# Performance work log

Measured on AMD Instinct MI355X. Metric: run time of the kernel, lower is better.

Reference implementation:

```python
import jax, jax.numpy as jnp
import numpy as np

T, B, D, H = 256, 64, 1024, 1024


def setup_inputs() -> dict:
    key = jax.random.key(0)
    ks = jax.random.split(key, 12)
    stdv = 1.0 / np.sqrt(H)
    u = lambda k, shape: jax.random.uniform(k, shape, jnp.float32, -stdv, stdv)
    return {
        "input_": jax.random.normal(ks[0], (T, B, D), jnp.float32),
        "length": jax.random.randint(ks[1], (B,), 1, T + 1, jnp.int32),
        "h0": jnp.zeros((B, H), jnp.float32),
        "cj": jax.random.normal(ks[2], (B, H), jnp.float32),
        "he": jax.random.normal(ks[3], (B, H), jnp.float32),
        "w_ih": u(ks[4], (3 * H, D)),
        "w_hh": u(ks[5], (3 * H, H)),
        "w_ch": u(ks[6], (3 * H, H)),
        "w_zh": u(ks[7], (3 * H, H)),
        "b_ih": u(ks[8], (3 * H,)),
        "b_hh": u(ks[9], (3 * H,)),
        "b_ch": u(ks[10], (3 * H,)),
        "b_zh": u(ks[11], (3 * H,)),
    }


def _chunk3(g):
    # mirrors torch .chunk(3, 1) on a (..., 3H) tensor
    return g[..., :H], g[..., H:2 * H], g[..., 2 * H:]


def reference(input_, length, h0, cj, he, w_ih, w_hh, w_ch, w_zh,
              b_ih, b_hh, b_ch, b_zh):
    # context projections are time-invariant: hoist out of the recurrence
    c_r, c_i, c_n = _chunk3(cj @ w_ch.T + b_ch)   # (B,H) each
    z_r, z_i, z_n = _chunk3(he @ w_zh.T + b_zh)   # (B,H) each
    # input projections for all steps at once: (T,B,3H)
    gi_all = jnp.einsum('tbd,gd->tbg', input_, w_ih) + b_ih

    def step(h, xs):
        gi_t, t = xs
        i_r, i_i, i_n = _chunk3(gi_t)
        h_r, h_i, h_n_ = _chunk3(h @ w_hh.T + b_hh)
        resetgate = jax.nn.sigmoid(i_r + h_r + c_r + z_r)
        inputgate = jax.nn.sigmoid(i_i + h_i + c_i + z_i)
        newgate = jnp.tanh(i_n + resetgate * h_n_ + c_n + z_n)
        hy = newgate + inputgate * (h - newgate)
        mask = (t < length).astype(hy.dtype)[:, None]          # (B,1)
        # NOTE: faithful to original torch code, which uses hx[0]
        # (first batch row, broadcast) in the masked branch.
        h_next = hy * mask + h[0] * (1.0 - mask)
        return h_next, h_next

    h_last, output = jax.lax.scan(step, h0, (gi_all, jnp.arange(T)))
    h_n = h_last[None]  # (num_layers=1, B, H)
    return output, h_n
```

## Files before the change

kernel.cpp:

```cpp
#include <hip/hip_runtime.h>
#include <stdint.h>

#define TT 256
#define BB 64
#define DD 1024
#define HH 1024
#define G3 3072

typedef unsigned long long ull;
typedef __attribute__((ext_vector_type(8))) short short8;
typedef __attribute__((ext_vector_type(4))) float f32x4;

__device__ __forceinline__ unsigned short f2bf(float f) {
  union { float f; unsigned int i; } v; v.f = f;
  unsigned int x = v.i;
  return (unsigned short)((x + 0x7fffu + ((x >> 16) & 1u)) >> 16);
}
__device__ __forceinline__ float bf2f(unsigned short u) {
  union { unsigned int i; float f; } v; v.i = ((unsigned int)u) << 16; return v.f;
}
__device__ __forceinline__ f32x4 mfma16(short8 a, short8 b, f32x4 c) {
  return __builtin_amdgcn_mfma_f32_16x16x32_bf16(a, b, c, 0, 0, 0);
}
__device__ __forceinline__ void gload_lds16(const void* g, void* l) {
  __builtin_amdgcn_global_load_lds((const __attribute__((address_space(1))) void*)g,
                                   (__attribute__((address_space(3))) void*)l,
                                   16, 0, 0);
}

__global__ void k_cvt_bf16(const float* __restrict__ in, unsigned short* __restrict__ out, int n4) {
  int i = blockIdx.x * blockDim.x + threadIdx.x;
  int stride = gridDim.x * blockDim.x;
  for (; i < n4; i += stride) {
    float4 v = ((const float4*)in)[i];
    ushort4 o;
    o.x = f2bf(v.x); o.y = f2bf(v.y); o.z = f2bf(v.z); o.w = f2bf(v.w);
    ((ushort4*)out)[i] = o;
  }
}

__global__ __launch_bounds__(256) void k_ctx(
    const unsigned short* __restrict__ cjb, const unsigned short* __restrict__ heb,
    const unsigned short* __restrict__ Wchb, const unsigned short* __restrict__ Wzhb,
    const float* __restrict__ b_ih, const float* __restrict__ b_hh,
    const float* __restrict__ b_ch, const float* __restrict__ b_zh,
    float* __restrict__ E) {
  __shared__ f32x4 red[4][4][64];
  int n0 = blockIdx.x * 16;
  int tid = threadIdx.x;
  int w = tid >> 6, l = tid & 63, lo = l & 15, hi = l >> 4;
  f32x4 acc[4];
#pragma unroll
  for (int r = 0; r < 4; r++) acc[r] = (f32x4){0.f, 0.f, 0.f, 0.f};
#pragma unroll 4
  for (int kk = 0; kk < 16; kk++) {
    int k = w * 512 + kk * 32;
    const unsigned short* Asrc = (k < 1024) ? cjb : heb;
    const unsigned short* Bsrc = (k < 1024) ? Wchb : Wzhb;
    int kw = (k < 1024) ? k : (k - 1024);
    int kof = kw + hi * 8;
    short8 bf = *(const short8*)(Bsrc + (size_t)(n0 + lo) * 1024 + kof);
#pragma unroll
    for (int r = 0; r < 4; r++) {
      short8 af = *(const short8*)(Asrc + (size_t)(r * 16 + lo) * 1024 + kof);
      acc[r] = mfma16(af, bf, acc[r]);
    }
  }
#pragma unroll
  for (int r = 0; r < 4; r++) red[w][r][l] = acc[r];
  __syncthreads();
  f32x4 s = red[0][w][l];
#pragma unroll
  for (int w2 = 1; w2 < 4; w2++) {
    f32x4 p = red[w2][w][l];
    s[0] += p[0]; s[1] += p[1]; s[2] += p[2]; s[3] += p[3];
  }
  int g = n0 + lo;
  float bias = b_ih[g] + b_ch[g] + b_zh[g] + ((g < 2048) ? b_hh[g] : 0.0f);
#pragma unroll
  for (int j = 0; j < 4; j++) {
    int b = w * 16 + hi * 4 + j;
    E[(size_t)b * G3 + g] = s[j] + bias;
  }
}

__global__ __launch_bounds__(256) void k_gemm_gi(
    const unsigned short* __restrict__ Xb,
    const unsigned short* __restrict__ Wb,
    const float* __restrict__ E,
    unsigned short* __restrict__ gi) {
  __shared__ unsigned short As[128 * 32];
  __shared__ unsigned short Bs[128 * 32];
  int bid = blockIdx.x;
  int mt = bid & 127;
  int nt = bid >> 7;
  int m0 = mt * 128, n0 = nt * 128;
  int tid = threadIdx.x;
  int w = tid >> 6, l = tid & 63, lo = l & 15, hi = l >> 4;
  int wr = w >> 1, wc = w & 1;
  f32x4 acc[4][4];
#pragma unroll
  for (int i = 0; i < 4; i++)
#pragma unroll
    for (int j = 0; j < 4; j++) acc[i][j] = (f32x4){0.f, 0.f, 0.f, 0.f};
  int srow = tid >> 2;
  int scol = (tid & 3) * 8;
  for (int kt = 0; kt < 32; kt++) {
    int k0 = kt * 32;
    __syncthreads();
    gload_lds16(Xb + (size_t)(m0 + srow) * 1024 + k0 + scol, As + srow * 32 + scol);
    gload_lds16(Xb + (size_t)(m0 + 64 + srow) * 1024 + k0 + scol, As + (64 + srow) * 32 + scol);
    gload_lds16(Wb + (size_t)(n0 + srow) * 1024 + k0 + scol, Bs + srow * 32 + scol);
    gload_lds16(Wb + (size_t)(n0 + 64 + srow) * 1024 + k0 + scol, Bs + (64 + srow) * 32 + scol);
    asm volatile("s_waitcnt vmcnt(0)" ::: "memory");
    __syncthreads();
    short8 a[4], b[4];
#pragma unroll
    for (int i = 0; i < 4; i++) a[i] = *(const short8*)(As + (wr * 64 + i * 16 + lo) * 32 + hi * 8);
#pragma unroll
    for (int i = 0; i < 4; i++) b[i] = *(const short8*)(Bs + (wc * 64 + i * 16 + lo) * 32 + hi * 8);
#pragma unroll
    for (int i = 0; i < 4; i++)
#pragma unroll
      for (int j = 0; j < 4; j++) acc[i][j] = mfma16(a[i], b[j], acc[i][j]);
  }
#pragma unroll
  for (int i = 0; i < 4; i++)
#pragma unroll
    for (int j = 0; j < 4; j++)
#pragma unroll
      for (int e = 0; e < 4; e++) {
        int r = m0 + wr * 64 + i * 16 + hi * 4 + e;
        int c = n0 + wc * 64 + j * 16 + lo;
        float v = acc[i][j][e] + E[(size_t)(r & 63) * G3 + c];
        gi[(size_t)r * G3 + c] = f2bf(v);
      }
}

__global__ __launch_bounds__(256) void k_rnn(
    const unsigned short* __restrict__ giE,
    const unsigned short* __restrict__ Whhb,
    const float* __restrict__ b_hh,
    const float* __restrict__ h0,
    const int* __restrict__ length,
    unsigned short* __restrict__ hbuf,
    float* __restrict__ out,
    float* __restrict__ hn,
    unsigned int* __restrict__ seq) {
  extern __shared__ char smem[];
  unsigned short* wlds = (unsigned short*)smem;
  f32x4* red = (f32x4*)(smem + 98304);
  float* hp0 = (float*)(smem + 98304 + 49152);

  const int cs = blockIdx.x;
  const int j0 = cs * 16;
  const int tid = threadIdx.x;
  const int kq = tid >> 6, l = tid & 63, lo = l & 15, hi = l >> 4;
  const int rowbase = kq * 16;
  const int col = j0 + lo;

#pragma unroll
  for (int kk = 0; kk < 8; ++kk)
#pragma unroll
    for (int s = 0; s < 3; ++s) {
      int f = (kq * 8 + kk) * 3 + s;
      short8 v = *(const short8*)(Whhb + (size_t)(s * 1024 + j0 + lo) * 1024 + kq * 256 + kk * 32 + hi * 8);
      ((short8*)wlds)[f * 64 + l] = v;
    }

  const float bhhn = b_hh[2048 + col];
  float hown[4];
  int len4[4];
#pragma unroll
  for (int j = 0; j < 4; ++j) {
    int b = rowbase + hi * 4 + j;
    hown[j] = h0[(size_t)b * 1024 + col];
    len4[j] = length[b];
  }
#pragma unroll
  for (int j = 0; j < 4; ++j) {
    unsigned int mine = f2bf(hown[j]);
    unsigned int oth = __shfl_xor(mine, 1, 64);
    if (!(lo & 1)) {
      int row = rowbase + hi * 4 + j;
      __hip_atomic_store((unsigned int*)(hbuf + (size_t)cs * 1024 + row * 16 + lo),
                         mine | (oth << 16), __ATOMIC_RELAXED, __HIP_MEMORY_SCOPE_AGENT);
    }
  }
  if (kq == 0 && hi == 0) hp0[lo] = hown[0];
  float gir[3][4];
#pragma unroll
  for (int s = 0; s < 3; ++s)
#pragma unroll
    for (int j = 0; j < 4; ++j)
      gir[s][j] = bf2f(giE[(size_t)(rowbase + hi * 4 + j) * G3 + s * 1024 + col]);
  __syncthreads();
  asm volatile("s_waitcnt vmcnt(0)" ::: "memory");
  if (l == 0)
    __hip_atomic_store(&seq[(cs * 4 + kq) * 16], 1u, __ATOMIC_RELAXED, __HIP_MEMORY_SCOPE_AGENT);

  int slot = 0;
  for (int t = 0; t < TT; ++t) {
    const int nslot = (slot == 2) ? 0 : slot + 1;
    {
      const unsigned int* sp = seq + ((size_t)(kq * 16 + (l >> 2)) * 4 + (l & 3)) * 16;
      unsigned int tgt = (unsigned int)(t + 1);
      for (;;) {
        unsigned int v = __hip_atomic_load(sp, __ATOMIC_RELAXED, __HIP_MEMORY_SCOPE_AGENT);
        if (__all(v >= tgt)) break;
        __builtin_amdgcn_s_sleep(1);
      }
    }
    const unsigned short* hb2 = hbuf + (size_t)slot * 65536;
    union AF { ull u[2]; short8 v; };
    AF a[4][8];
#pragma unroll
    for (int rt = 0; rt < 4; ++rt)
#pragma unroll
      for (int kk = 0; kk < 8; ++kk) {
        int k = kq * 256 + kk * 32;
        int blk = (k >> 4) + (hi >> 1);
        const unsigned short* hp = hb2 + (size_t)blk * 1024 + (rt * 16 + lo) * 16 + (hi & 1) * 8;
        a[rt][kk].u[0] = __hip_atomic_load((const ull*)hp, __ATOMIC_RELAXED, __HIP_MEMORY_SCOPE_AGENT);
        a[rt][kk].u[1] = __hip_atomic_load((const ull*)hp + 1, __ATOMIC_RELAXED, __HIP_MEMORY_SCOPE_AGENT);
      }
    f32x4 acc[4][3];
#pragma unroll
    for (int rt = 0; rt < 4; ++rt)
#pragma unroll
      for (int s = 0; s < 3; ++s) acc[rt][s] = (f32x4){0.f, 0.f, 0.f, 0.f};
#pragma unroll
    for (int kk = 0; kk < 8; ++kk) {
      const short8* wf = ((const short8*)wlds) + (size_t)((kq * 8 + kk) * 3) * 64 + l;
      short8 b0 = wf[0];
      short8 b1 = wf[64];
      short8 b2 = wf[128];
#pragma unroll
      for (int rt = 0; rt < 4; ++rt) {
        acc[rt][0] = mfma16(a[rt][kk].v, b0, acc[rt][0]);
        acc[rt][1] = mfma16(a[rt][kk].v, b1, acc[rt][1]);
        acc[rt][2] = mfma16(a[rt][kk].v, b2, acc[rt][2]);
      }
    }
#pragma unroll
    for (int rt = 0; rt < 4; ++rt)
#pragma unroll
      for (int s = 0; s < 3; ++s)
        red[((size_t)kq * 12 + rt * 3 + s) * 64 + l] = acc[rt][s];
    __syncthreads();
    f32x4 fin[3];
#pragma unroll
    for (int s = 0; s < 3; ++s) {
      f32x4 v = red[((size_t)0 * 12 + kq * 3 + s) * 64 + l];
#pragma unroll
      for (int q = 1; q < 4; ++q) {
        f32x4 p = red[((size_t)q * 12 + kq * 3 + s) * 64 + l];
        v[0] += p[0]; v[1] += p[1]; v[2] += p[2]; v[3] += p[3];
      }
      fin[s] = v;
    }
    float h0p = hp0[(t & 1) * 16 + lo];
    __syncthreads();
    float hv[4];
#pragma unroll
    for (int j = 0; j < 4; ++j) {
      float R = fin[0][j] + gir[0][j];
      float I = fin[1][j] + gir[1][j];
      float rg = 1.f / (1.f + __expf(-R));
      float ig = 1.f / (1.f + __expf(-I));
      float nx = gir[2][j] + rg * (fin[2][j] + bhhn);
      nx = fminf(15.f, fmaxf(-15.f, nx));
      float e2 = __expf(2.f * nx);
      float ng = (e2 - 1.f) / (e2 + 1.f);
      float hy = ng + ig * (hown[j] - ng);
      float res = (t < len4[j]) ? hy : h0p;
      hv[j] = res;
      hown[j] = res;
    }
    if (t < TT - 1) {
      unsigned short* dst = hbuf + (size_t)nslot * 65536 + (size_t)cs * 1024;
#pragma unroll
      for (int j = 0; j < 4; ++j) {
        unsigned int mine = f2bf(hv[j]);
        unsigned int oth = __shfl_xor(mine, 1, 64);
        if (!(lo & 1)) {
          int row = rowbase + hi * 4 + j;
          __hip_atomic_store((unsigned int*)(dst + row * 16 + lo),
                             mine | (oth << 16), __ATOMIC_RELAXED, __HIP_MEMORY_SCOPE_AGENT);
        }
      }
      if (kq == 0 && hi == 0) hp0[((t + 1) & 1) * 16 + lo] = hv[0];
      asm volatile("s_waitcnt vmcnt(0)" ::: "memory");
      if (l == 0)
        __hip_atomic_store(&seq[(cs * 4 + kq) * 16], (unsigned int)(t + 2),
                           __ATOMIC_RELAXED, __HIP_MEMORY_SCOPE_AGENT);
    }
#pragma unroll
    for (int j = 0; j < 4; ++j) {
      int b = rowbase + hi * 4 + j;
      out[(size_t)t * (BB * HH) + (size_t)b * 1024 + col] = hv[j];
    }
    if (t == TT - 1) {
#pragma unroll
      for (int j = 0; j < 4; ++j) {
        int b = rowbase + hi * 4 + j;
        hn[(size_t)b * 1024 + col] = hv[j];
      }
    } else {
      const unsigned short* gb = giE + (size_t)(t + 1) * 64 * G3;
#pragma unroll
      for (int s = 0; s < 3; ++s)
#pragma unroll
        for (int j = 0; j < 4; ++j)
          gir[s][j] = bf2f(gb[(size_t)(rowbase + hi * 4 + j) * G3 + s * 1024 + col]);
    }
    slot = nslot;
  }
}

extern "C" void kernel_launch(void* const* d_in, const int* in_sizes, int n_in,
                              void* d_out, int out_size, void* d_ws, size_t ws_size,
                              hipStream_t stream) {
  const float* input_ = (const float*)d_in[0];
  const int* length   = (const int*)d_in[1];
  const float* h0     = (const float*)d_in[2];
  const float* cj     = (const float*)d_in[3];
  const float* he     = (const float*)d_in[4];
  const float* w_ih   = (const float*)d_in[5];
  const float* w_hh   = (const float*)d_in[6];
  const float* w_ch   = (const float*)d_in[7];
  const float* w_zh   = (const float*)d_in[8];
  const float* b_ih   = (const float*)d_in[9];
  const float* b_hh   = (const float*)d_in[10];
  const float* b_ch   = (const float*)d_in[11];
  const float* b_zh   = (const float*)d_in[12];

  char* ws = (char*)d_ws;
  const size_t OFF_SEQ   = 0;
  const size_t OFF_XB    = 131072;
  const size_t OFF_WIHB  = OFF_XB + 33554432ull;
  const size_t OFF_WHHB  = OFF_WIHB + 6291456ull;
  const size_t OFF_WCHB  = OFF_WHHB + 6291456ull;
  const size_t OFF_WZHB  = OFF_WCHB + 6291456ull;
  const size_t OFF_CJB   = OFF_WZHB + 6291456ull;
  const size_t OFF_HEB   = OFF_CJB + 131072ull;
  const size_t OFF_E     = OFF_HEB + 131072ull;
  const size_t OFF_GI    = OFF_E + 786432ull;
  const size_t OFF_HBUF  = OFF_GI + 100663296ull;

  unsigned int* seq     = (unsigned int*)(ws + OFF_SEQ);
  unsigned short* Xb    = (unsigned short*)(ws + OFF_XB);
  unsigned short* Wihb  = (unsigned short*)(ws + OFF_WIHB);
  unsigned short* Whhb  = (unsigned short*)(ws + OFF_WHHB);
  unsigned short* Wchb  = (unsigned short*)(ws + OFF_WCHB);
  unsigned short* Wzhb  = (unsigned short*)(ws + OFF_WZHB);
  unsigned short* cjb   = (unsigned short*)(ws + OFF_CJB);
  unsigned short* heb   = (unsigned short*)(ws + OFF_HEB);
  float* E              = (float*)(ws + OFF_E);
  unsigned short* gi    = (unsigned short*)(ws + OFF_GI);
  unsigned short* hbuf  = (unsigned short*)(ws + OFF_HBUF);

  float* out = (float*)d_out;
  float* hn  = out + 16777216;

  hipFuncSetAttribute((const void*)k_rnn, hipFuncAttributeMaxDynamicSharedMemorySize, 147584);

  hipMemsetAsync(seq, 0, 16384, stream);
  k_cvt_bf16<<<2048, 256, 0, stream>>>(input_, Xb, 16777216 / 4);
  k_cvt_bf16<<<1024, 256, 0, stream>>>(w_ih, Wihb, 3145728 / 4);
  k_cvt_bf16<<<1024, 256, 0, stream>>>(w_hh, Whhb, 3145728 / 4);
  k_cvt_bf16<<<1024, 256, 0, stream>>>(w_ch, Wchb, 3145728 / 4);
  k_cvt_bf16<<<1024, 256, 0, stream>>>(w_zh, Wzhb, 3145728 / 4);
  k_cvt_bf16<<<64, 256, 0, stream>>>(cj, cjb, 65536 / 4);
  k_cvt_bf16<<<64, 256, 0, stream>>>(he, heb, 65536 / 4);
  k_ctx<<<192, 256, 0, stream>>>(cjb, heb, Wchb, Wzhb, b_ih, b_hh, b_ch, b_zh, E);
  k_gemm_gi<<<3072, 256, 0, stream>>>(Xb, Wihb, E, gi);
  k_rnn<<<64, 256, 147584, stream>>>(gi, Whhb, b_hh, h0, length, hbuf, out, hn, seq);
}
```

Baseline: 1.454 ms.

## Warp-specialize RNN kernel with helper waves for gi prefetch and output stores

Doubles the recurrent kernel's block to 512 threads. Four helper waves prefetch the next step's gate inputs into a double-buffered LDS area and write the per-step outputs, reading them back from the bf16 hidden-state exchange buffer two steps late. This takes global gi loads and output stores off the serial critical path of the update waves. The h-exchange loads switch from relaxed atomic 64-bit loads to inline-asm dwordx4 loads with sc0 sc1 cache bits. In exchange, intermediate outputs are now bf16-rounded rather than the fp32 values, and there are more waves per barrier.

```diff
diff --git a/kernel.cpp b/kernel.cpp
--- a/kernel.cpp
+++ b/kernel.cpp
@@ -26,6 +26,11 @@
   __builtin_amdgcn_global_load_lds((const __attribute__((address_space(1))) void*)g,
                                    (__attribute__((address_space(3))) void*)l,
                                    16, 0, 0);
+}
+__device__ __forceinline__ short8 mall_load16(const unsigned short* p) {
+  short8 r;
+  asm volatile("global_load_dwordx4 %0, %1, off sc0 sc1" : "=v"(r) : "v"(p));
+  return r;
 }
 
 __global__ void k_cvt_bf16(const float* __restrict__ in, unsigned short* __restrict__ out, int n4) {
@@ -137,7 +142,7 @@
       }
 }
 
-__global__ __launch_bounds__(256) void k_rnn(
+__global__ __launch_bounds__(512) void k_rnn(
     const unsigned short* __restrict__ giE,
     const unsigned short* __restrict__ Whhb,
     const float* __restrict__ b_hh,
@@ -150,59 +155,71 @@
   extern __shared__ char smem[];
   unsigned short* wlds = (unsigned short*)smem;
   f32x4* red = (f32x4*)(smem + 98304);
-  float* hp0 = (float*)(smem + 98304 + 49152);
+  unsigned short* giL = (unsigned short*)(smem + 147456);
+  float* hp0 = (float*)(smem + 160512);
 
   const int cs = blockIdx.x;
   const int j0 = cs * 16;
   const int tid = threadIdx.x;
-  const int kq = tid >> 6, l = tid & 63, lo = l & 15, hi = l >> 4;
+  const int w = tid >> 6, l = tid & 63, lo = l & 15, hi = l >> 4;
+  const bool is_upd = (w < 4);
+  const int kq = w & 3;
   const int rowbase = kq * 16;
   const int col = j0 + lo;
 
-#pragma unroll
-  for (int kk = 0; kk < 8; ++kk)
-#pragma unroll
-    for (int s = 0; s < 3; ++s) {
-      int f = (kq * 8 + kk) * 3 + s;
-      short8 v = *(const short8*)(Whhb + (size_t)(s * 1024 + j0 + lo) * 1024 + kq * 256 + kk * 32 + hi * 8);
-      ((short8*)wlds)[f * 64 + l] = v;
-    }
-
-  const float bhhn = b_hh[2048 + col];
-  float hown[4];
-  int len4[4];
-#pragma unroll
-  for (int j = 0; j < 4; ++j) {
-    int b = rowbase + hi * 4 + j;
-    hown[j] = h0[(size_t)b * 1024 + col];
-    len4[j] = length[b];
-  }
-#pragma unroll
-  for (int j = 0; j < 4; ++j) {
-    unsigned int mine = f2bf(hown[j]);
-    unsigned int oth = __shfl_xor(mine, 1, 64);
-    if (!(lo & 1)) {
-      int row = rowbase + hi * 4 + j;
-      __hip_atomic_store((unsigned int*)(hbuf + (size_t)cs * 1024 + row * 16 + lo),
-                         mine | (oth << 16), __ATOMIC_RELAXED, __HIP_MEMORY_SCOPE_AGENT);
-    }
-  }
-  if (kq == 0 && hi == 0) hp0[lo] = hown[0];
-  float gir[3][4];
-#pragma unroll
-  for (int s = 0; s < 3; ++s)
-#pragma unroll
-    for (int j = 0; j < 4; ++j)
-      gir[s][j] = bf2f(giE[(size_t)(rowbase + hi * 4 + j) * G3 + s * 1024 + col]);
+  float bhhn = 0.f;
+  float hown[4] = {0.f, 0.f, 0.f, 0.f};
+  int len4[4] = {0, 0, 0, 0};
+
+  if (is_upd) {
+#pragma unroll
+    for (int kk = 0; kk < 8; ++kk)
+#pragma unroll
+      for (int s = 0; s < 3; ++s) {
+        int f = (kq * 8 + kk) * 3 + s;
+        short8 v = *(const short8*)(Whhb + (size_t)(s * 1024 + j0 + lo) * 1024 + kq * 256 + kk * 32 + hi * 8);
+        ((short8*)wlds)[f * 64 + l] = v;
+      }
+    bhhn = b_hh[2048 + col];
+#pragma unroll
+    for (int j = 0; j < 4; ++j) {
+      int b = rowbase + hi * 4 + j;
+      hown[j] = h0[(size_t)b * 1024 + col];
+      len4[j] = length[b];
+    }
+#pragma unroll
+    for (int j = 0; j < 4; ++j) {
+      unsigned int mine = f2bf(hown[j]);
+      unsigned int oth = __shfl_xor(mine, 1, 64);
+      if (!(lo & 1)) {
+        int row = rowbase + hi * 4 + j;
+        __hip_atomic_store((unsigned int*)(hbuf + (size_t)cs * 1024 + row * 16 + lo),
+                           mine | (oth << 16), __ATOMIC_RELAXED, __HIP_MEMORY_SCOPE_AGENT);
+      }
+    }
+    if (kq == 0 && hi == 0) hp0[lo] = hown[0];
+  } else {
+#pragma unroll
+    for (int s = 0; s < 3; ++s)
+#pragma unroll
+      for (int j = 0; j < 4; ++j) {
+        int b = rowbase + hi * 4 + j;
+        giL[(size_t)(0 * 64 + b) * 51 + s * 17 + lo] =
+            giE[(size_t)b * G3 + s * 1024 + col];
+      }
+  }
   __syncthreads();
-  asm volatile("s_waitcnt vmcnt(0)" ::: "memory");
-  if (l == 0)
-    __hip_atomic_store(&seq[(cs * 4 + kq) * 16], 1u, __ATOMIC_RELAXED, __HIP_MEMORY_SCOPE_AGENT);
+  if (is_upd) {
+    asm volatile("s_waitcnt vmcnt(0)" ::: "memory");
+    if (l == 0)
+      __hip_atomic_store(&seq[(cs * 4 + kq) * 16], 1u, __ATOMIC_RELAXED, __HIP_MEMORY_SCOPE_AGENT);
+  }
 
   int slot = 0;
   for (int t = 0; t < TT; ++t) {
     const int nslot = (slot == 2) ? 0 : slot + 1;
-    {
+    unsigned short gval[12];
+    if (is_upd) {
       const unsigned int* sp = seq + ((size_t)(kq * 16 + (l >> 2)) * 4 + (l & 3)) * 16;
       unsigned int tgt = (unsigned int)(t + 1);
       for (;;) {
@@ -210,111 +227,151 @@
         if (__all(v >= tgt)) break;
         __builtin_amdgcn_s_sleep(1);
       }
-    }
-    const unsigned short* hb2 = hbuf + (size_t)slot * 65536;
-    union AF { ull u[2]; short8 v; };
-    AF a[4][8];
-#pragma unroll
-    for (int rt = 0; rt < 4; ++rt)
+      const unsigned short* hb2 = hbuf + (size_t)slot * 65536;
+      short8 a[4][8];
+#pragma unroll
+      for (int rt = 0; rt < 4; ++rt)
+#pragma unroll
+        for (int kk = 0; kk < 8; ++kk) {
+          int blk = kq * 16 + kk * 2 + (hi >> 1);
+          a[rt][kk] = mall_load16(hb2 + (size_t)blk * 1024 + (rt * 16 + lo) * 16 + (hi & 1) * 8);
+        }
+      asm volatile("s_waitcnt vmcnt(0)" ::: "memory");
+      __builtin_amdgcn_sched_barrier(0);
+      f32x4 acc[4][3];
+#pragma unroll
+      for (int rt = 0; rt < 4; ++rt)
+#pragma unroll
+        for (int s = 0; s < 3; ++s) acc[rt][s] = (f32x4){0.f, 0.f, 0.f, 0.f};
 #pragma unroll
       for (int kk = 0; kk < 8; ++kk) {
-        int k = kq * 256 + kk * 32;
-        int blk = (k >> 4) + (hi >> 1);
-        const unsigned short* hp = hb2 + (size_t)blk * 1024 + (rt * 16 + lo) * 16 + (hi & 1) * 8;
-        a[rt][kk].u[0] = __hip_atomic_load((const ull*)hp, __ATOMIC_RELAXED, __HIP_MEMORY_SCOPE_AGENT);
-        a[rt][kk].u[1] = __hip_atomic_load((const ull*)hp + 1, __ATOMIC_RELAXED, __HIP_MEMORY_SCOPE_AGENT);
-      }
-    f32x4 acc[4][3];
-#pragma unroll
-    for (int rt = 0; rt < 4; ++rt)
-#pragma unroll
-      for (int s = 0; s < 3; ++s) acc[rt][s] = (f32x4){0.f, 0.f, 0.f, 0.f};
-#pragma unroll
-    for (int kk = 0; kk < 8; ++kk) {
-      const short8* wf = ((const short8*)wlds) + (size_t)((kq * 8 + kk) * 3) * 64 + l;
-      short8 b0 = wf[0];
-      short8 b1 = wf[64];
-      short8 b2 = wf[128];
-#pragma unroll
-      for (int rt = 0; rt < 4; ++rt) {
-        acc[rt][0] = mfma16(a[rt][kk].v, b0, acc[rt][0]);
-        acc[rt][1] = mfma16(a[rt][kk].v, b1, acc[rt][1]);
-        acc[rt][2] = mfma16(a[rt][kk].v, b2, acc[rt][2]);
-      }
-    }
-#pragma unroll
-    for (int rt = 0; rt < 4; ++rt)
-#pragma unroll
-      for (int s = 0; s < 3; ++s)
-        red[((size_t)kq * 12 + rt * 3 + s) * 64 + l] = acc[rt][s];
+        const short8* wf = ((const short8*)wlds) + (size_t)((kq * 8 + kk) * 3) * 64 + l;
+        short8 b0 = wf[0];
+        short8 b1 = wf[64];
+        short8 b2 = wf[128];
+#pragma unroll
+        for (int rt = 0; rt < 4; ++rt) {
+          acc[rt][0] = mfma16(a[rt][kk], b0, acc[rt][0]);
+          acc[rt][1] = mfma16(a[rt][kk], b1, acc[rt][1]);
+          acc[rt][2] = mfma16(a[rt][kk], b2, acc[rt][2]);
+        }
+      }
+#pragma unroll
+      for (int rt = 0; rt < 4; ++rt)
+#pragma unroll
+        for (int s = 0; s < 3; ++s)
+          red[((size_t)kq * 12 + rt * 3 + s) * 64 + l] = acc[rt][s];
+    } else {
+      if (t >= 2) {
+        const unsigned short* hblk = hbuf + (size_t)((t + 2) % 3) * 65536 + (size_t)cs * 1024;
+        int row = rowbase + (l >> 2);
+        int c4 = (l & 3) * 4;
+        ull d = __hip_atomic_load((const ull*)(hblk + row * 16 + c4),
+                                  __ATOMIC_RELAXED, __HIP_MEMORY_SCOPE_AGENT);
+        float4 o;
+        o.x = bf2f((unsigned short)d);
+        o.y = bf2f((unsigned short)(d >> 16));
+        o.z = bf2f((unsigned short)(d >> 32));
+        o.w = bf2f((unsigned short)(d >> 48));
+        *(float4*)(out + (size_t)(t - 2) * (BB * HH) + (size_t)row * 1024 + j0 + c4) = o;
+      }
+      if (t < TT - 1) {
+        const unsigned short* gb = giE + (size_t)(t + 1) * 64 * G3;
+#pragma unroll
+        for (int s = 0; s < 3; ++s)
+#pragma unroll
+          for (int j = 0; j < 4; ++j)
+            gval[s * 4 + j] = gb[(size_t)(rowbase + hi * 4 + j) * G3 + s * 1024 + col];
+      }
+    }
     __syncthreads();
     f32x4 fin[3];
-#pragma unroll
-    for (int s = 0; s < 3; ++s) {
-      f32x4 v = red[((size_t)0 * 12 + kq * 3 + s) * 64 + l];
-#pragma unroll
-      for (int q = 1; q < 4; ++q) {
-        f32x4 p = red[((size_t)q * 12 + kq * 3 + s) * 64 + l];
-        v[0] += p[0]; v[1] += p[1]; v[2] += p[2]; v[3] += p[3];
-      }
-      fin[s] = v;
-    }
-    float h0p = hp0[(t & 1) * 16 + lo];
+    float h0p = 0.f;
+    if (is_upd) {
+#pragma unroll
+      for (int s = 0; s < 3; ++s) {
+        f32x4 v = red[((size_t)0 * 12 + kq * 3 + s) * 64 + l];
+#pragma unroll
+        for (int q = 1; q < 4; ++q) {
+          f32x4 p = red[((size_t)q * 12 + kq * 3 + s) * 64 + l];
+          v[0] += p[0]; v[1] += p[1]; v[2] += p[2]; v[3] += p[3];
+        }
+        fin[s] = v;
+      }
+      h0p = hp0[(t & 1) * 16 + lo];
+    } else if (t < TT - 1) {
+#pragma unroll
+      for (int s = 0; s < 3; ++s)
+#pragma unroll
+        for (int j = 0; j < 4; ++j) {
+          int b = rowbase + hi * 4 + j;
+          giL[(size_t)(((t + 1) & 1) * 64 + b) * 51 + s * 17 + lo] = gval[s * 4 + j];
+        }
+    }
     __syncthreads();
-    float hv[4];
-#pragma unroll
-    for (int j = 0; j < 4; ++j) {
-      float R = fin[0][j] + gir[0][j];
-      float I = fin[1][j] + gir[1][j];
-      float rg = 1.f / (1.f + __expf(-R));
-      float ig = 1.f / (1.f + __expf(-I));
-      float nx = gir[2][j] + rg * (fin[2][j] + bhhn);
-      nx = fminf(15.f, fmaxf(-15.f, nx));
-      float e2 = __expf(2.f * nx);
-      float ng = (e2 - 1.f) / (e2 + 1.f);
-      float hy = ng + ig * (hown[j] - ng);
-      float res = (t < len4[j]) ? hy : h0p;
-      hv[j] = res;
-      hown[j] = res;
-    }
-    if (t < TT - 1) {
-      unsigned short* dst = hbuf + (size_t)nslot * 65536 + (size_t)cs * 1024;
+    if (is_upd) {
+      float gir_sj;
+      float hv[4];
 #pragma unroll
       for (int j = 0; j < 4; ++j) {
-        unsigned int mine = f2bf(hv[j]);
-        unsigned int oth = __shfl_xor(mine, 1, 64);
-        if (!(lo & 1)) {
-          int row = rowbase + hi * 4 + j;
-          __hip_atomic_store((unsigned int*)(dst + row * 16 + lo),
-                             mine | (oth << 16), __ATOMIC_RELAXED, __HIP_MEMORY_SCOPE_AGENT);
+        int b = rowbase + hi * 4 + j;
+        float g0 = bf2f(giL[(size_t)((t & 1) * 64 + b) * 51 + 0 * 17 + lo]);
+        float g1 = bf2f(giL[(size_t)((t & 1) * 64 + b) * 51 + 1 * 17 + lo]);
+        float g2 = bf2f(giL[(size_t)((t & 1) * 64 + b) * 51 + 2 * 17 + lo]);
+        float R = fin[0][j] + g0;
+        float I = fin[1][j] + g1;
+        float rg = 1.f / (1.f + __expf(-R));
+        float ig = 1.f / (1.f + __expf(-I));
+        float nx = g2 + rg * (fin[2][j] + bhhn);
+        nx = fminf(15.f, fmaxf(-15.f, nx));
+        float e2 = __expf(2.f * nx);
+        float ng = (e2 - 1.f) / (e2 + 1.f);
+        float hy = ng + ig * (hown[j] - ng);
+        float res = (t < len4[j]) ? hy : h0p;
+        hv[j] = res;
+        hown[j] = res;
+      }
+      (void)gir_sj;
+      if (t < TT - 1) {
+        unsigned short* dst = hbuf + (size_t)nslot * 65536 + (size_t)cs * 1024;
+#pragma unroll
+        for (int j = 0; j < 4; ++j) {
+          unsigned int mine = f2bf(hv[j]);
+          unsigned int oth = __shfl_xor(mine, 1, 64);
+          if (!(lo & 1)) {
+            int row = rowbase + hi * 4 + j;
+            __hip_atomic_store((unsigned int*)(dst + row * 16 + lo),
+                               mine | (oth << 16), __ATOMIC_RELAXED, __HIP_MEMORY_SCOPE_AGENT);
+          }
         }
-      }
-      if (kq == 0 && hi == 0) hp0[((t + 1) & 1) * 16 + lo] = hv[0];
-      asm volatile("s_waitcnt vmcnt(0)" ::: "memory");
-      if (l == 0)
-        __hip_atomic_store(&seq[(cs * 4 + kq) * 16], (unsigned int)(t + 2),
-                           __ATOMIC_RELAXED, __HIP_MEMORY_SCOPE_AGENT);
-    }
+        if (kq == 0 && hi == 0) hp0[((t + 1) & 1) * 16 + lo] = hv[0];
+        asm volatile("s_waitcnt vmcnt(0)" ::: "memory");
+        if (l == 0)
+          __hip_atomic_store(&seq[(cs * 4 + kq) * 16], (unsigned int)(t + 2),
+                             __ATOMIC_RELAXED, __HIP_MEMORY_SCOPE_AGENT);
+      }
+    }
+    slot = nslot;
+  }
+  if (is_upd) {
 #pragma unroll
     for (int j = 0; j < 4; ++j) {
       int b = rowbase + hi * 4 + j;
-      out[(size_t)t * (BB * HH) + (size_t)b * 1024 + col] = hv[j];
-    }
-    if (t == TT - 1) {
-#pragma unroll
-      for (int j = 0; j < 4; ++j) {
-        int b = rowbase + hi * 4 + j;
-        hn[(size_t)b * 1024 + col] = hv[j];
-      }
-    } else {
-      const unsigned short* gb = giE + (size_t)(t + 1) * 64 * G3;
-#pragma unroll
-      for (int s = 0; s < 3; ++s)
-#pragma unroll
-        for (int j = 0; j < 4; ++j)
-          gir[s][j] = bf2f(gb[(size_t)(rowbase + hi * 4 + j) * G3 + s * 1024 + col]);
-    }
-    slot = nslot;
+      out[(size_t)(TT - 1) * (BB * HH) + (size_t)b * 1024 + col] = hown[j];
+      hn[(size_t)b * 1024 + col] = hown[j];
+    }
+  } else {
+    const unsigned short* hblk = hbuf + (size_t)((TT - 1) % 3) * 65536 + (size_t)cs * 1024;
+    int row = rowbase + (l >> 2);
+    int c4 = (l & 3) * 4;
+    ull d = __hip_atomic_load((const ull*)(hblk + row * 16 + c4),
+                              __ATOMIC_RELAXED, __HIP_MEMORY_SCOPE_AGENT);
+    float4 o;
+    o.x = bf2f((unsigned short)d);
+    o.y = bf2f((unsigned short)(d >> 16));
+    o.z = bf2f((unsigned short)(d >> 32));
+    o.w = bf2f((unsigned short)(d >> 48));
+    *(float4*)(out + (size_t)(TT - 2) * (BB * HH) + (size_t)row * 1024 + j0 + c4) = o;
   }
 }
 
@@ -363,7 +420,7 @@
   float* out = (float*)d_out;
   float* hn  = out + 16777216;
 
-  hipFuncSetAttribute((const void*)k_rnn, hipFuncAttributeMaxDynamicSharedMemorySize, 147584);
+  hipFuncSetAttribute((const void*)k_rnn, hipFuncAttributeMaxDynamicSharedMemorySize, 160640);
 
   hipMemsetAsync(seq, 0, 16384, stream);
   k_cvt_bf16<<<2048, 256, 0, stream>>>(input_, Xb, 16777216 / 4);
@@ -375,5 +432,5 @@
   k_cvt_bf16<<<64, 256, 0, stream>>>(he, heb, 65536 / 4);
   k_ctx<<<192, 256, 0, stream>>>(cjb, heb, Wchb, Wzhb, b_ih, b_hh, b_ch, b_zh, E);
   k_gemm_gi<<<3072, 256, 0, stream>>>(Xb, Wihb, E, gi);
-  k_rnn<<<64, 256, 147584, stream>>>(gi, Whhb, b_hh, h0, length, hbuf, out, hn, seq);
-}
+  k_rnn<<<64, 512, 160640, stream>>>(gi, Whhb, b_hh, h0, length, hbuf, out, hn, seq);
+}
```

Measured after the change: 1.444 ms. No clear change (-0.7%).

## Pipeline recurrent step across four batch groups with per-group sync

Applied to the files above, without the earlier changes.

Splits each timestep of the persistent GRU kernel into four phases, one per 16-row batch group. Each group's hidden-state slice is published with its own sequence counter, so the next group's poll and h loads overlap the current group's MFMA and gate math instead of waiting on a full-step barrier. The hidden-state buffer moves to a compact per-group double-buffered layout at the start of the workspace and is read with sc0/sc1 cache-bypass loads. The cost is four times as many barriers and polls per step, and the memory-ordering assumptions are subtle.

```diff
diff --git a/kernel.cpp b/kernel.cpp
--- a/kernel.cpp
+++ b/kernel.cpp
@@ -26,6 +26,11 @@
   __builtin_amdgcn_global_load_lds((const __attribute__((address_space(1))) void*)g,
                                    (__attribute__((address_space(3))) void*)l,
                                    16, 0, 0);
+}
+__device__ __forceinline__ short8 mall_load16(const unsigned short* p) {
+  short8 r;
+  asm volatile("global_load_dwordx4 %0, %1, off sc0 sc1" : "=v"(r) : "v"(p));
+  return r;
 }
 
 __global__ void k_cvt_bf16(const float* __restrict__ in, unsigned short* __restrict__ out, int n4) {
@@ -150,13 +155,11 @@
   extern __shared__ char smem[];
   unsigned short* wlds = (unsigned short*)smem;
   f32x4* red = (f32x4*)(smem + 98304);
-  float* hp0 = (float*)(smem + 98304 + 49152);
-
-  const int cs = blockIdx.x;
-  const int j0 = cs * 16;
+  float* h0f = (float*)(smem + 98304 + 24576);
+
+  const int cs = blockIdx.x, j0 = cs * 16;
   const int tid = threadIdx.x;
   const int kq = tid >> 6, l = tid & 63, lo = l & 15, hi = l >> 4;
-  const int rowbase = kq * 16;
   const int col = j0 + lo;
 
 #pragma unroll
@@ -173,149 +176,158 @@
   int len4[4];
 #pragma unroll
   for (int j = 0; j < 4; ++j) {
-    int b = rowbase + hi * 4 + j;
+    int b = kq * 16 + hi * 4 + j;
     hown[j] = h0[(size_t)b * 1024 + col];
     len4[j] = length[b];
   }
-#pragma unroll
-  for (int j = 0; j < 4; ++j) {
-    unsigned int mine = f2bf(hown[j]);
-    unsigned int oth = __shfl_xor(mine, 1, 64);
-    if (!(lo & 1)) {
-      int row = rowbase + hi * 4 + j;
-      __hip_atomic_store((unsigned int*)(hbuf + (size_t)cs * 1024 + row * 16 + lo),
-                         mine | (oth << 16), __ATOMIC_RELAXED, __HIP_MEMORY_SCOPE_AGENT);
+  {
+    unsigned short* dst = hbuf + ((size_t)(kq * 2 + 0) * 64 + cs) * 256;
+#pragma unroll
+    for (int j = 0; j < 4; ++j) {
+      unsigned int mine = f2bf(hown[j]);
+      unsigned int oth = __shfl_xor(mine, 1, 64);
+      if (!(lo & 1))
+        __hip_atomic_store((unsigned int*)(dst + (hi * 4 + j) * 16 + lo),
+                           mine | (oth << 16), __ATOMIC_RELAXED, __HIP_MEMORY_SCOPE_AGENT);
     }
   }
-  if (kq == 0 && hi == 0) hp0[lo] = hown[0];
-  float gir[3][4];
+  if (kq == 0 && hi == 0) h0f[0 * 16 + lo] = hown[0];
+  unsigned short girP[12];
 #pragma unroll
   for (int s = 0; s < 3; ++s)
 #pragma unroll
     for (int j = 0; j < 4; ++j)
-      gir[s][j] = bf2f(giE[(size_t)(rowbase + hi * 4 + j) * G3 + s * 1024 + col]);
+      girP[s * 4 + j] = giE[(size_t)(kq * 16 + hi * 4 + j) * G3 + s * 1024 + col];
   __syncthreads();
   asm volatile("s_waitcnt vmcnt(0)" ::: "memory");
   if (l == 0)
     __hip_atomic_store(&seq[(cs * 4 + kq) * 16], 1u, __ATOMIC_RELAXED, __HIP_MEMORY_SCOPE_AGENT);
 
-  int slot = 0;
-  for (int t = 0; t < TT; ++t) {
-    const int nslot = (slot == 2) ? 0 : slot + 1;
-    {
-      const unsigned int* sp = seq + ((size_t)(kq * 16 + (l >> 2)) * 4 + (l & 3)) * 16;
-      unsigned int tgt = (unsigned int)(t + 1);
-      for (;;) {
-        unsigned int v = __hip_atomic_load(sp, __ATOMIC_RELAXED, __HIP_MEMORY_SCOPE_AGENT);
-        if (__all(v >= tgt)) break;
-        __builtin_amdgcn_s_sleep(1);
-      }
-    }
-    const unsigned short* hb2 = hbuf + (size_t)slot * 65536;
-    union AF { ull u[2]; short8 v; };
-    AF a[4][8];
-#pragma unroll
-    for (int rt = 0; rt < 4; ++rt)
-#pragma unroll
-      for (int kk = 0; kk < 8; ++kk) {
-        int k = kq * 256 + kk * 32;
-        int blk = (k >> 4) + (hi >> 1);
-        const unsigned short* hp = hb2 + (size_t)blk * 1024 + (rt * 16 + lo) * 16 + (hi & 1) * 8;
-        a[rt][kk].u[0] = __hip_atomic_load((const ull*)hp, __ATOMIC_RELAXED, __HIP_MEMORY_SCOPE_AGENT);
-        a[rt][kk].u[1] = __hip_atomic_load((const ull*)hp + 1, __ATOMIC_RELAXED, __HIP_MEMORY_SCOPE_AGENT);
-      }
-    f32x4 acc[4][3];
-#pragma unroll
-    for (int rt = 0; rt < 4; ++rt)
-#pragma unroll
-      for (int s = 0; s < 3; ++s) acc[rt][s] = (f32x4){0.f, 0.f, 0.f, 0.f};
-#pragma unroll
-    for (int kk = 0; kk < 8; ++kk) {
-      const short8* wf = ((const short8*)wlds) + (size_t)((kq * 8 + kk) * 3) * 64 + l;
-      short8 b0 = wf[0];
-      short8 b1 = wf[64];
-      short8 b2 = wf[128];
-#pragma unroll
-      for (int rt = 0; rt < 4; ++rt) {
-        acc[rt][0] = mfma16(a[rt][kk].v, b0, acc[rt][0]);
-        acc[rt][1] = mfma16(a[rt][kk].v, b1, acc[rt][1]);
-        acc[rt][2] = mfma16(a[rt][kk].v, b2, acc[rt][2]);
-      }
-    }
-#pragma unroll
-    for (int rt = 0; rt < 4; ++rt)
-#pragma unroll
-      for (int s = 0; s < 3; ++s)
-        red[((size_t)kq * 12 + rt * 3 + s) * 64 + l] = acc[rt][s];
-    __syncthreads();
-    f32x4 fin[3];
-#pragma unroll
-    for (int s = 0; s < 3; ++s) {
-      f32x4 v = red[((size_t)0 * 12 + kq * 3 + s) * 64 + l];
-#pragma unroll
-      for (int q = 1; q < 4; ++q) {
-        f32x4 p = red[((size_t)q * 12 + kq * 3 + s) * 64 + l];
-        v[0] += p[0]; v[1] += p[1]; v[2] += p[2]; v[3] += p[3];
-      }
-      fin[s] = v;
-    }
-    float h0p = hp0[(t & 1) * 16 + lo];
-    __syncthreads();
-    float hv[4];
-#pragma unroll
-    for (int j = 0; j < 4; ++j) {
-      float R = fin[0][j] + gir[0][j];
-      float I = fin[1][j] + gir[1][j];
-      float rg = 1.f / (1.f + __expf(-R));
-      float ig = 1.f / (1.f + __expf(-I));
-      float nx = gir[2][j] + rg * (fin[2][j] + bhhn);
-      nx = fminf(15.f, fmaxf(-15.f, nx));
-      float e2 = __expf(2.f * nx);
-      float ng = (e2 - 1.f) / (e2 + 1.f);
-      float hy = ng + ig * (hown[j] - ng);
-      float res = (t < len4[j]) ? hy : h0p;
-      hv[j] = res;
-      hown[j] = res;
-    }
-    if (t < TT - 1) {
-      unsigned short* dst = hbuf + (size_t)nslot * 65536 + (size_t)cs * 1024;
-#pragma unroll
-      for (int j = 0; j < 4; ++j) {
-        unsigned int mine = f2bf(hv[j]);
-        unsigned int oth = __shfl_xor(mine, 1, 64);
-        if (!(lo & 1)) {
-          int row = rowbase + hi * 4 + j;
-          __hip_atomic_store((unsigned int*)(dst + row * 16 + lo),
-                             mine | (oth << 16), __ATOMIC_RELAXED, __HIP_MEMORY_SCOPE_AGENT);
-        }
-      }
-      if (kq == 0 && hi == 0) hp0[((t + 1) & 1) * 16 + lo] = hv[0];
-      asm volatile("s_waitcnt vmcnt(0)" ::: "memory");
-      if (l == 0)
-        __hip_atomic_store(&seq[(cs * 4 + kq) * 16], (unsigned int)(t + 2),
-                           __ATOMIC_RELAXED, __HIP_MEMORY_SCOPE_AGENT);
-    }
-#pragma unroll
-    for (int j = 0; j < 4; ++j) {
-      int b = rowbase + hi * 4 + j;
-      out[(size_t)t * (BB * HH) + (size_t)b * 1024 + col] = hv[j];
-    }
-    if (t == TT - 1) {
-#pragma unroll
-      for (int j = 0; j < 4; ++j) {
-        int b = rowbase + hi * 4 + j;
-        hn[(size_t)b * 1024 + col] = hv[j];
-      }
-    } else {
-      const unsigned short* gb = giE + (size_t)(t + 1) * 64 * G3;
-#pragma unroll
-      for (int s = 0; s < 3; ++s)
-#pragma unroll
-        for (int j = 0; j < 4; ++j)
-          gir[s][j] = bf2f(gb[(size_t)(rowbase + hi * 4 + j) * G3 + s * 1024 + col]);
-    }
-    slot = nslot;
-  }
+  short8 aE[8], aO[8];
+
+#define POLL_ISSUE(GNX, TNX, AN)                                                        \
+  {                                                                                     \
+    const unsigned int* sp = seq + ((size_t)(kq * 16 + (l & 15)) * 4 + (GNX)) * 16;     \
+    unsigned int tgt = (unsigned int)((TNX) + 1);                                       \
+    for (;;) {                                                                          \
+      unsigned int v = __hip_atomic_load(sp, __ATOMIC_RELAXED, __HIP_MEMORY_SCOPE_AGENT);\
+      if (__all(v >= tgt)) break;                                                       \
+      __builtin_amdgcn_s_sleep(1);                                                      \
+    }                                                                                   \
+    const unsigned short* base = hbuf + ((size_t)((GNX) * 2 + ((TNX) & 1)) * 64) * 256; \
+    _Pragma("unroll")                                                                   \
+    for (int kk = 0; kk < 8; ++kk) {                                                    \
+      int blk = kq * 16 + kk * 2 + (hi >> 1);                                           \
+      AN[kk] = mall_load16(base + (size_t)blk * 256 + lo * 16 + (hi & 1) * 8);          \
+    }                                                                                   \
+    if ((GNX) == kq && (TNX) < TT) {                                                    \
+      const unsigned short* gb = giE + (size_t)(TNX) * 64 * G3;                         \
+      _Pragma("unroll")                                                                 \
+      for (int s = 0; s < 3; ++s)                                                       \
+        _Pragma("unroll")                                                               \
+        for (int j = 0; j < 4; ++j)                                                     \
+          girP[s * 4 + j] = gb[(size_t)(kq * 16 + hi * 4 + j) * G3 + s * 1024 + col];   \
+    }                                                                                   \
+  }
+
+#define PHASE(P, AC, AN)                                                                \
+  {                                                                                     \
+    const int g = (P) & 3;                                                              \
+    const int t = (P) >> 2;                                                             \
+    const int par = (P) & 1;                                                            \
+    asm volatile("s_waitcnt vmcnt(0)" ::: "memory");                                    \
+    __builtin_amdgcn_sched_barrier(0);                                                  \
+    f32x4 ac0 = {0.f, 0.f, 0.f, 0.f}, ac1 = ac0, ac2 = ac0;                             \
+    _Pragma("unroll")                                                                   \
+    for (int kk = 0; kk < 8; ++kk) {                                                    \
+      const short8* wf = ((const short8*)wlds) + (size_t)((kq * 8 + kk) * 3) * 64 + l;  \
+      short8 b0 = wf[0];                                                                \
+      short8 b1 = wf[64];                                                               \
+      short8 b2 = wf[128];                                                              \
+      ac0 = mfma16(AC[kk], b0, ac0);                                                    \
+      ac1 = mfma16(AC[kk], b1, ac1);                                                    \
+      ac2 = mfma16(AC[kk], b2, ac2);                                                    \
+    }                                                                                   \
+    red[((size_t)(par * 4 + kq) * 3 + 0) * 64 + l] = ac0;                               \
+    red[((size_t)(par * 4 + kq) * 3 + 1) * 64 + l] = ac1;                               \
+    red[((size_t)(par * 4 + kq) * 3 + 2) * 64 + l] = ac2;                               \
+    if ((P) + 1 < 4 * TT) {                                                             \
+      const int gnx = ((P) + 1) & 3, tnx = ((P) + 1) >> 2;                              \
+      POLL_ISSUE(gnx, tnx, AN);                                                         \
+    }                                                                                   \
+    asm volatile("s_waitcnt lgkmcnt(0)" ::: "memory");                                  \
+    __builtin_amdgcn_s_barrier();                                                       \
+    __builtin_amdgcn_sched_barrier(0);                                                  \
+    if (kq == g) {                                                                      \
+      f32x4 fin[3];                                                                     \
+      _Pragma("unroll")                                                                 \
+      for (int s = 0; s < 3; ++s) {                                                     \
+        f32x4 v = red[((size_t)(par * 4 + 0) * 3 + s) * 64 + l];                        \
+        _Pragma("unroll")                                                               \
+        for (int q = 1; q < 4; ++q) {                                                   \
+          f32x4 pp = red[((size_t)(par * 4 + q) * 3 + s) * 64 + l];                     \
+          v[0] += pp[0]; v[1] += pp[1]; v[2] += pp[2]; v[3] += pp[3];                   \
+        }                                                                               \
+        fin[s] = v;                                                                     \
+      }                                                                                 \
+      float h0p = (g == 0) ? __shfl(hown[0], lo, 64) : h0f[(t & 3) * 16 + lo];          \
+      float hv[4];                                                                      \
+      _Pragma("unroll")                                                                 \
+      for (int j = 0; j < 4; ++j) {                                                     \
+        float R = fin[0][j] + bf2f(girP[0 * 4 + j]);                                    \
+        float I = fin[1][j] + bf2f(girP[1 * 4 + j]);                                    \
+        float rg = 1.f / (1.f + __expf(-R));                                            \
+        float ig = 1.f / (1.f + __expf(-I));                                            \
+        float nx = bf2f(girP[2 * 4 + j]) + rg * (fin[2][j] + bhhn);                     \
+        nx = fminf(15.f, fmaxf(-15.f, nx));                                             \
+        float e2 = __expf(2.f * nx);                                                    \
+        float ng = (e2 - 1.f) / (e2 + 1.f);                                             \
+        float hy = ng + ig * (hown[j] - ng);                                            \
+        float res = (t < len4[j]) ? hy : h0p;                                           \
+        hv[j] = res;                                                                    \
+        hown[j] = res;                                                                  \
+      }                                                                                 \
+      if (t < TT - 1) {                                                                 \
+        unsigned short* dst = hbuf + ((size_t)(g * 2 + ((t + 1) & 1)) * 64 + cs) * 256; \
+        _Pragma("unroll")                                                               \
+        for (int j = 0; j < 4; ++j) {                                                   \
+          unsigned int mine = f2bf(hv[j]);                                              \
+          unsigned int oth = __shfl_xor(mine, 1, 64);                                   \
+          if (!(lo & 1))                                                                \
+            __hip_atomic_store((unsigned int*)(dst + (hi * 4 + j) * 16 + lo),           \
+                               mine | (oth << 16), __ATOMIC_RELAXED,                    \
+                               __HIP_MEMORY_SCOPE_AGENT);                               \
+        }                                                                               \
+        if (g == 0 && hi == 0) h0f[((t + 1) & 3) * 16 + lo] = hv[0];                    \
+        asm volatile("s_waitcnt vmcnt(0)" ::: "memory");                                \
+        if (l == 0)                                                                     \
+          __hip_atomic_store(&seq[(cs * 4 + g) * 16], (unsigned int)(t + 2),            \
+                             __ATOMIC_RELAXED, __HIP_MEMORY_SCOPE_AGENT);               \
+        _Pragma("unroll")                                                               \
+        for (int j = 0; j < 4; ++j) {                                                   \
+          int b = g * 16 + hi * 4 + j;                                                  \
+          out[(size_t)t * (BB * HH) + (size_t)b * 1024 + col] = hv[j];                  \
+        }                                                                               \
+      } else {                                                                          \
+        _Pragma("unroll")                                                               \
+        for (int j = 0; j < 4; ++j) {                                                   \
+          int b = g * 16 + hi * 4 + j;                                                  \
+          out[(size_t)t * (BB * HH) + (size_t)b * 1024 + col] = hv[j];                  \
+          hn[(size_t)b * 1024 + col] = hv[j];                                           \
+        }                                                                               \
+      }                                                                                 \
+    }                                                                                   \
+  }
+
+  POLL_ISSUE(0, 0, aE);
+
+  for (int p2 = 0; p2 < 2 * TT; ++p2) {
+    int p = p2 * 2;
+    PHASE(p, aE, aO);
+    PHASE(p + 1, aO, aE);
+  }
+#undef PHASE
+#undef POLL_ISSUE
 }
 
 extern "C" void kernel_launch(void* const* d_in, const int* in_sizes, int n_in,
@@ -337,7 +349,8 @@
 
   char* ws = (char*)d_ws;
   const size_t OFF_SEQ   = 0;
-  const size_t OFF_XB    = 131072;
+  const size_t OFF_HBUF  = 16384;
+  const size_t OFF_XB    = 524288;
   const size_t OFF_WIHB  = OFF_XB + 33554432ull;
   const size_t OFF_WHHB  = OFF_WIHB + 6291456ull;
   const size_t OFF_WCHB  = OFF_WHHB + 6291456ull;
@@ -346,9 +359,9 @@
   const size_t OFF_HEB   = OFF_CJB + 131072ull;
   const size_t OFF_E     = OFF_HEB + 131072ull;
   const size_t OFF_GI    = OFF_E + 786432ull;
-  const size_t OFF_HBUF  = OFF_GI + 100663296ull;
 
   unsigned int* seq     = (unsigned int*)(ws + OFF_SEQ);
+  unsigned short* hbuf  = (unsigned short*)(ws + OFF_HBUF);
   unsigned short* Xb    = (unsigned short*)(ws + OFF_XB);
   unsigned short* Wihb  = (unsigned short*)(ws + OFF_WIHB);
   unsigned short* Whhb  = (unsigned short*)(ws + OFF_WHHB);
@@ -358,12 +371,11 @@
   unsigned short* heb   = (unsigned short*)(ws + OFF_HEB);
   float* E              = (float*)(ws + OFF_E);
   unsigned short* gi    = (unsigned short*)(ws + OFF_GI);
-  unsigned short* hbuf  = (unsigned short*)(ws + OFF_HBUF);
 
   float* out = (float*)d_out;
   float* hn  = out + 16777216;
 
-  hipFuncSetAttribute((const void*)k_rnn, hipFuncAttributeMaxDynamicSharedMemorySize, 147584);
+  hipFuncSetAttribute((const void*)k_rnn, hipFuncAttributeMaxDynamicSharedMemorySize, 123136);
 
   hipMemsetAsync(seq, 0, 16384, stream);
   k_cvt_bf16<<<2048, 256, 0, stream>>>(input_, Xb, 16777216 / 4);
@@ -375,5 +387,5 @@
   k_cvt_bf16<<<64, 256, 0, stream>>>(he, heb, 65536 / 4);
   k_ctx<<<192, 256, 0, stream>>>(cjb, heb, Wchb, Wzhb, b_ih, b_hh, b_ch, b_zh, E);
   k_gemm_gi<<<3072, 256, 0, stream>>>(Xb, Wihb, E, gi);
-  k_rnn<<<64, 256, 147584, stream>>>(gi, Whhb, b_hh, h0, length, hbuf, out, hn, seq);
-}
+  k_rnn<<<64, 256, 123136, stream>>>(gi, Whhb, b_hh, h0, length, hbuf, out, hn, seq);
+}
```

Result: slower. 2.891 ms (+98.8%).
